# Performance work log

Measured on AMD Instinct MI355X. Metric: run time of the kernel, lower is better.

The kernel has to match this reference:

```python
import jax, jax.numpy as jnp
import numpy as np

NUM_BOXES = 16384
NUM_CLASS = 3
CODE_SIZE = 7
NMS_PRE = 1024
NMS_POST = 512
NMS_THRESH = 0.8
EPS = 1e-8


def _cross(a, b):
    return a[..., 0] * b[..., 1] - a[..., 1] * b[..., 0]


def _bev_corners(b5):
    # b5: (..., 5) = (cx, cy, dx, dy, ry) -> corners (..., 4, 2)
    c, s = jnp.cos(b5[..., 4]), jnp.sin(b5[..., 4])
    off = jnp.array([[0.5, 0.5], [-0.5, 0.5], [-0.5, -0.5], [0.5, -0.5]], dtype=b5.dtype)
    lx = b5[..., 2:3] * off[:, 0]  # (..., 4)
    ly = b5[..., 3:4] * off[:, 1]
    cx = b5[..., 0:1] + lx * c[..., None] - ly * s[..., None]
    cy = b5[..., 1:2] + lx * s[..., None] + ly * c[..., None]
    return jnp.stack([cx, cy], axis=-1)


def _points_in_box(p, b5):
    # p: (..., K, 2), b5: (..., 5) -> (..., K) bool (point inside rotated rect)
    c, s = jnp.cos(b5[..., 4:5]), jnp.sin(b5[..., 4:5])
    rel = p - b5[..., None, 0:2]
    qx = rel[..., 0] * c + rel[..., 1] * s
    qy = -rel[..., 0] * s + rel[..., 1] * c
    return (jnp.abs(qx) <= b5[..., 2:3] * 0.5 + 1e-5) & (jnp.abs(qy) <= b5[..., 3:4] * 0.5 + 1e-5)


def _pairwise_bev_iou(b5):
    # b5: (N, 5) -> (N, N) rotated BEV IoU (matches iou3d nms_gpu's BEV IoU)
    a = b5[:, None, :]
    b = b5[None, :, :]
    ca = _bev_corners(a)  # (N,1,4,2)
    cb = _bev_corners(b)  # (1,N,4,2)
    # edge-edge segment intersections: (N,N,4,4)
    a0, da = ca, jnp.roll(ca, -1, axis=-2) - ca
    b0, db = cb, jnp.roll(cb, -1, axis=-2) - cb
    A0, DA = a0[..., :, None, :], da[..., :, None, :]
    B0, DB = b0[..., None, :, :], db[..., None, :, :]
    den = _cross(DA, DB)
    d = B0 - A0
    den_s = jnp.where(jnp.abs(den) > EPS, den, 1.0)
    t = _cross(d, DB) / den_s
    u = _cross(d, DA) / den_s
    ok = (jnp.abs(den) > EPS) & (t >= 0) & (t <= 1) & (u >= 0) & (u <= 1)
    p_ee = A0 + t[..., None] * DA  # (N,N,4,4,2)
    shp = p_ee.shape[:-3]
    p_ee = p_ee.reshape(shp + (16, 2))
    ok = ok.reshape(shp + (16,))
    in_b = _points_in_box(ca, b)  # corners of A inside B: (N,N,4)
    in_a = _points_in_box(cb, a)  # corners of B inside A: (N,N,4)
    pts = jnp.concatenate([p_ee,
                           jnp.broadcast_to(ca, shp + (4, 2)),
                           jnp.broadcast_to(cb, shp + (4, 2))], axis=-2)  # (N,N,24,2)
    msk = jnp.concatenate([ok, in_b, in_a], axis=-1)  # (N,N,24)
    # order candidate vertices by angle around centroid (intersection is convex)
    cnt = jnp.maximum(msk.sum(-1, keepdims=True), 1)
    ctr = (pts * msk[..., None]).sum(-2, keepdims=True) / cnt[..., None]  # (N,N,1,2)
    ang = jnp.arctan2(pts[..., 1] - ctr[..., 1], pts[..., 0] - ctr[..., 0])
    ang = jnp.where(msk, ang, 1e9)  # invalid points sorted to the end
    order = jnp.argsort(ang, axis=-1)
    pts_s = jnp.take_along_axis(pts, order[..., None], axis=-2)
    msk_s = jnp.take_along_axis(msk, order, axis=-1)
    first = pts_s[..., 0:1, :]
    poly = jnp.where(msk_s[..., None], pts_s, first)  # pad with first vertex (zero shoelace contribution)
    inter = 0.5 * jnp.abs(_cross(poly, jnp.roll(poly, -1, axis=-2)).sum(-1))
    area_a = a[..., 2] * a[..., 3]
    area_b = b[..., 2] * b[..., 3]
    return inter / jnp.maximum(area_a + area_b - inter, 1e-6)


def _greedy_nms(iou, thresh):
    n = iou.shape[0]
    idx = jnp.arange(n)

    def body(i, supp):
        alive = jnp.logical_not(supp[i])
        return supp | (alive & (iou[i] > thresh) & (idx > i))

    supp = jax.lax.fori_loop(0, n, body, jnp.zeros((n,), dtype=bool))
    return ~supp


def _select_one(box_preds, cls_preds):
    # box_preds: (M, 7), cls_preds: (M, C) -> padded selected indices + validity
    scores = jnp.max(cls_preds, axis=1)
    _, top_idx = jax.lax.top_k(scores, NMS_PRE)  # score-descending, like torch.topk
    bev = box_preds[top_idx][:, jnp.array([0, 1, 3, 4, 6])]  # (cx,cy,dx,dy,ry)
    iou = _pairwise_bev_iou(bev)
    keep = _greedy_nms(iou, NMS_THRESH)
    pri = jnp.where(keep, jnp.arange(NMS_PRE), 2 * NMS_PRE)
    pos = jnp.sort(pri)[:NMS_POST]  # kept positions in score order
    valid = pos < NMS_PRE
    sel = top_idx[jnp.minimum(pos, NMS_PRE - 1)]
    return sel, valid


def setup_inputs() -> dict:
    key = jax.random.key(0)
    k1, k2, k3, k4, k5 = jax.random.split(key, 5)
    B = 2
    xy = jax.random.uniform(k1, (B, NUM_BOXES, 2), minval=-50.0, maxval=50.0)
    z = jax.random.uniform(k2, (B, NUM_BOXES, 1), minval=-2.0, maxval=1.0)
    dims = jax.random.uniform(k3, (B, NUM_BOXES, 3), minval=1.0, maxval=5.0)
    ry = jax.random.uniform(k4, (B, NUM_BOXES, 1), minval=-np.pi, maxval=np.pi)
    batch_box_preds = jnp.concatenate([xy, z, dims, ry], axis=-1).astype(jnp.float32)
    batch_cls_preds = (jax.random.normal(k5, (B, NUM_BOXES, NUM_CLASS)) * 3.0).astype(jnp.float32)
    return {"batch_box_preds": batch_box_preds, "batch_cls_preds": batch_cls_preds}


def reference(batch_box_preds, batch_cls_preds):
    # RoIHeadTemplate.proposal_layer: per-sample max-score, class-agnostic NMS,
    # scatter into zero-padded (B, NMS_POST, ...) tensors.
    sel, valid = jax.vmap(_select_one)(batch_box_preds, batch_cls_preds)  # (B, NMS_POST)
    rois = jnp.take_along_axis(batch_box_preds, sel[..., None], axis=1)
    logits = jnp.take_along_axis(batch_cls_preds, sel[..., None], axis=1)
    labels = jnp.argmax(logits, axis=-1)
    scores = jnp.max(logits, axis=-1)
    v = valid[..., None]
    rois = jnp.where(v, rois, 0.0)
    logits = jnp.where(v, logits, 0.0)
    scores = jnp.where(valid, scores, 0.0)
    roi_labels = jnp.where(valid, labels, 0) + 1  # padded slots end up as 1, same as torch (zeros + 1)
    return rois, scores, roi_labels, logits
```

## Files before the change

### kernel.cpp

```cpp
#include <hip/hip_runtime.h>
#include <hip/hip_bf16.h>
#include <math.h>

#define NBOX   16384
#define NPRE   1024
#define NPOST  512
#define NMS_TH 0.8f
#define DEN_EPS 1e-8f
#define NCAND  2048
#define NBUCK  8192
#define SEGCAP 16384
#define CANDL  2048

typedef unsigned long long ull;

__device__ __forceinline__ unsigned mono_f32(float a) {
  unsigned u = __float_as_uint(a);
  return (u & 0x80000000u) ? ~u : (u | 0x80000000u);
}

__global__ __launch_bounds__(256) void k_sel(
    const float* __restrict__ cls, ull* __restrict__ cand,
    unsigned* __restrict__ candCnt) {
  __shared__ unsigned hist[NBUCK];
  __shared__ unsigned smallu[8];
  __shared__ unsigned thrT, cntL;
  const int b = blockIdx.x >> 3, s = blockIdx.x & 7;
  const int t = threadIdx.x;
  const int lane = t & 63, wv = t >> 6;
  const float* cb = cls + (size_t)b * NBOX * 3;

#pragma unroll
  for (int k = 0; k < NBUCK / 256; ++k) hist[t + k * 256] = 0u;
  if (t == 0) cntL = 0u;
  __syncthreads();

  for (int k = 0; k < 64; ++k) {
    int i = k * 256 + t;
    float sc = fmaxf(cb[i * 3], fmaxf(cb[i * 3 + 1], cb[i * 3 + 2]));
    atomicAdd(&hist[mono_f32(sc) >> 19], 1u);
  }
  __syncthreads();

  unsigned csum = 0;
#pragma unroll 8
  for (int k = 0; k < 32; ++k) csum += hist[t * 32 + k];
  unsigned v = csum;
#pragma unroll
  for (int off = 1; off < 64; off <<= 1) {
    unsigned o = __shfl_down((int)v, off, 64);
    if (lane + off < 64) v += o;
  }
  if (lane == 0) smallu[wv] = v;
  __syncthreads();
  unsigned shi = 0;
  for (int w2 = wv + 1; w2 < 4; ++w2) shi += smallu[w2];
  unsigned incl = v + shi;
  unsigned safter = incl - csum;
  if (safter < NPRE && incl >= NPRE) {
    unsigned c = safter;
    for (int k = 31; k >= 0; --k) {
      c += hist[t * 32 + k];
      if (c >= NPRE) { thrT = (unsigned)(t * 32 + k); break; }
    }
  }
  __syncthreads();
  unsigned T = thrT;

  ull* seg = cand + ((size_t)b * 8 + s) * 2048;
  for (int k = s * 8; k < s * 8 + 8; ++k) {
    int i = k * 256 + t;
    float sc = fmaxf(cb[i * 3], fmaxf(cb[i * 3 + 1], cb[i * 3 + 2]));
    unsigned u = mono_f32(sc);
    bool cnd = (u >> 19) >= T;
    ull bal = __ballot(cnd);
    if (bal) {
      unsigned base = 0;
      if (lane == 0) base = atomicAdd(&cntL, (unsigned)__popcll(bal));
      base = (unsigned)__shfl((int)base, 0, 64);
      if (cnd) {
        unsigned pos = base + (unsigned)__popcll(bal & ((1ull << lane) - 1ull));
        seg[pos] = (((ull)u) << 14) | (ull)(16383 - i);
      }
    }
  }
  __syncthreads();
  if (t == 0) candCnt[b * 8 + s] = cntL;
}

__global__ __launch_bounds__(256) void k_rank(
    const float* __restrict__ box, const ull* __restrict__ cand,
    const unsigned* __restrict__ candCnt,
    int* __restrict__ topi, float* __restrict__ binfo, float4* __restrict__ pinfoG) {
  __shared__ ull candL[NCAND];
  __shared__ unsigned offs[9];
  const int b = blockIdx.x >> 3, g = blockIdx.x & 7;
  const int t = threadIdx.x;

  if (t == 0) {
    unsigned o = 0;
    for (int s = 0; s < 8; ++s) {
      offs[s] = o;
      unsigned c = candCnt[b * 8 + s];
      o += (c < 2048u) ? c : 2048u;
    }
    offs[8] = o;
  }
  __syncthreads();
  unsigned C = offs[8]; if (C > NCAND) C = NCAND;
  for (int s = 0; s < 8; ++s) {
    unsigned base = offs[s], cnt = offs[s + 1] - offs[s];
    const ull* seg = cand + ((size_t)b * 8 + s) * 2048;
    for (unsigned e = (unsigned)t; e < cnt; e += 256) {
      unsigned dst = base + e;
      if (dst < NCAND) candL[dst] = seg[e];
    }
  }
  if (t < 2 && C + t < NCAND) candL[C + t] = 0ull;
  __syncthreads();

  int j = g * 256 + t;
  ull my = ((unsigned)j < C) ? candL[j] : 0ull;
  int r = 0;
  int kmax = (int)((C + 1) >> 1);
  const ulonglong2* p2 = (const ulonglong2*)candL;
  for (int k = 0; k < kmax; ++k) {
    ulonglong2 kk = p2[k];
    r += (kk.x > my) ? 1 : 0;
    r += (kk.y > my) ? 1 : 0;
  }
  if ((unsigned)j >= C || r >= NPRE) return;
  int i = 16383 - (int)(my & 0x3FFFULL);
  topi[b * NPRE + r] = i;
  const float* bp = box + ((size_t)b * NBOX + i) * 7;
  float x = bp[0], y = bp[1], dx = bp[3], dy = bp[4], ry = bp[6];
  float c = cosf(ry), s = sinf(ry);
  float* o = binfo + ((size_t)b * NPRE + r) * 16;
  o[0] = x; o[1] = y; o[2] = dx; o[3] = dy; o[4] = c; o[5] = s;
  const float offx[4] = {0.5f, -0.5f, -0.5f, 0.5f};
  const float offy[4] = {0.5f, 0.5f, -0.5f, -0.5f};
#pragma unroll
  for (int k = 0; k < 4; ++k) {
    float lx = dx * offx[k], ly = dy * offy[k];
    o[6 + k]  = x + lx * c - ly * s;
    o[10 + k] = y + lx * s + ly * c;
  }
  float rad = 0.5f * sqrtf(dx * dx + dy * dy);
  float area = dx * dy;
  o[14] = rad; o[15] = area;
  pinfoG[(size_t)b * NPRE + r] = make_float4(x, y, rad, area);
}

__device__ bool iou_exact_gt(const float* __restrict__ Ab, const float* __restrict__ Bb) {
  float ax = Ab[0], ay = Ab[1], bx = Bb[0], by = Bb[1];
  float aA = Ab[15], aB = Bb[15];
  float acx[4], acy[4], bcx[4], bcy[4];
#pragma unroll
  for (int k = 0; k < 4; ++k) {
    acx[k] = Ab[6 + k]; acy[k] = Ab[10 + k];
    bcx[k] = Bb[6 + k]; bcy[k] = Bb[10 + k];
  }
  float px[24], py[24];
  bool act[24];
#pragma unroll
  for (int p = 0; p < 4; ++p) {
    float A0x = acx[p], A0y = acy[p];
    float DAx = acx[(p + 1) & 3] - A0x, DAy = acy[(p + 1) & 3] - A0y;
#pragma unroll
    for (int q = 0; q < 4; ++q) {
      float B0x = bcx[q], B0y = bcy[q];
      float DBx = bcx[(q + 1) & 3] - B0x, DBy = bcy[(q + 1) & 3] - B0y;
      float den = DAx * DBy - DAy * DBx;
      float dxx = B0x - A0x, dyy = B0y - A0y;
      bool dok = fabsf(den) > DEN_EPS;
      float dens = dok ? den : 1.0f;
      float t = (dxx * DBy - dyy * DBx) / dens;
      float u = (dxx * DAy - dyy * DAx) / dens;
      int k = p * 4 + q;
      px[k] = A0x + t * DAx;
      py[k] = A0y + t * DAy;
      act[k] = dok && t >= 0.f && t <= 1.f && u >= 0.f && u <= 1.f;
    }
  }
  float cA = Ab[4], sA = Ab[5], cB = Bb[4], sB = Bb[5];
#pragma unroll
  for (int k = 0; k < 4; ++k) {
    float rx = acx[k] - bx, ry = acy[k] - by;
    float qx =  rx * cB + ry * sB, qy = -rx * sB + ry * cB;
    px[16 + k] = acx[k]; py[16 + k] = acy[k];
    act[16 + k] = (fabsf(qx) <= Bb[2] * 0.5f + 1e-5f) && (fabsf(qy) <= Bb[3] * 0.5f + 1e-5f);
  }
#pragma unroll
  for (int k = 0; k < 4; ++k) {
    float rx = bcx[k] - ax, ry = bcy[k] - ay;
    float qx =  rx * cA + ry * sA, qy = -rx * sA + ry * cA;
    px[20 + k] = bcx[k]; py[20 + k] = bcy[k];
    act[20 + k] = (fabsf(qx) <= Ab[2] * 0.5f + 1e-5f) && (fabsf(qy) <= Ab[3] * 0.5f + 1e-5f);
  }
  int cnt = 0; float sx = 0.f, sy = 0.f;
#pragma unroll
  for (int k = 0; k < 24; ++k)
    if (act[k]) { cnt++; sx += px[k]; sy += py[k]; }
  float fc = (float)(cnt > 1 ? cnt : 1);
  float cx0 = sx / fc, cy0 = sy / fc;
  ull key[24];
#pragma unroll
  for (int k = 0; k < 24; ++k) {
    float ang = atan2f(py[k] - cy0, px[k] - cx0);
    key[k] = act[k] ? ((((ull)mono_f32(ang)) << 5) | (ull)k) : ~0ull;
  }
  ull kmin = ~0ull; float fx = 0.f, fy = 0.f;
#pragma unroll
  for (int k = 0; k < 24; ++k) {
    bool lt = key[k] < kmin;
    kmin = lt ? key[k] : kmin;
    fx = lt ? px[k] : fx;
    fy = lt ? py[k] : fy;
  }
  float ssum = 0.f;
#pragma unroll
  for (int k = 0; k < 24; ++k) {
    ull myk = key[k];
    ull best = ~0ull; float nx = fx, ny = fy;
#pragma unroll
    for (int j = 0; j < 24; ++j) {
      bool c = (key[j] > myk) && (key[j] < best);
      best = c ? key[j] : best;
      nx = c ? px[j] : nx;
      ny = c ? py[j] : ny;
    }
    float contrib = px[k] * ny - py[k] * nx;
    ssum += (myk != ~0ull) ? contrib : 0.f;
  }
  float inter = 0.5f * fabsf(ssum);
  float uni = aA + aB - inter;
  return inter / fmaxf(uni, 1e-6f) > NMS_TH;
}

__global__ __launch_bounds__(256) void k_pairs(
    const float4* __restrict__ pinfoG, const float* __restrict__ binfo,
    unsigned* __restrict__ hitseg, unsigned* __restrict__ hitcnt) {
  __shared__ float4 pin[NPRE];
  __shared__ unsigned candL[CANDL];
  __shared__ unsigned cntC, cntH;
  const int b = blockIdx.x >> 6, blk = blockIdx.x & 63;
  const int t = threadIdx.x;
  const int lane = t & 63, wv = t >> 6;
#pragma unroll
  for (int k = 0; k < 4; ++k) pin[k * 256 + t] = pinfoG[(size_t)b * NPRE + k * 256 + t];
  if (t == 0) { cntC = 0u; cntH = 0u; }
  __syncthreads();

  const float* bi = binfo + (size_t)b * NPRE * 16;
  unsigned sbase = ((unsigned)b * 64 + (unsigned)blk) * SEGCAP;
  for (int iter = 0; iter < 64; ++iter) {
    int task = iter * 4 + wv;
    int q = task >> 4, w = task & 15;
    int i = q * 64 + blk;
    if (w * 64 + 63 <= i) continue;
    int j = w * 64 + lane;
    float4 pi = pin[i];
    float4 pj = pin[j];
    bool cnd = false;
    if (j > i) {
      float ddx = pi.x - pj.x, ddy = pi.y - pj.y;
      float rr = pi.z + pj.z + 1e-3f;
      if (ddx * ddx + ddy * ddy <= rr * rr) {
        float mn = fminf(pi.w, pj.w), mx = fmaxf(pi.w, pj.w);
        if (mn > NMS_TH * mx) cnd = true;
      }
    }
    ull bal = __ballot(cnd);
    if (!bal) continue;
    unsigned base = 0;
    if (lane == 0) base = atomicAdd(&cntC, (unsigned)__popcll(bal));
    base = (unsigned)__shfl((int)base, 0, 64);
    if (cnd) {
      unsigned off = base + (unsigned)__popcll(bal & ((1ull << lane) - 1ull));
      unsigned pk = ((unsigned)i << 10) | (unsigned)j;
      if (off < CANDL) candL[off] = pk;
      else {
        if (iou_exact_gt(bi + (size_t)i * 16, bi + (size_t)j * 16)) {
          unsigned h = atomicAdd(&cntH, 1u);
          hitseg[sbase + h] = pk;
        }
      }
    }
  }
  __syncthreads();

  unsigned C = cntC; if (C > CANDL) C = CANDL;
  for (unsigned e = (unsigned)t; e < C; e += 256) {
    unsigned pk = candL[e];
    unsigned i = pk >> 10, j = pk & 1023u;
    if (iou_exact_gt(bi + (size_t)i * 16, bi + (size_t)j * 16)) {
      unsigned h = atomicAdd(&cntH, 1u);
      hitseg[sbase + h] = pk;
    }
  }
  __syncthreads();
  if (t == 0) hitcnt[b * 64 + blk] = (cntH < (unsigned)SEGCAP) ? cntH : (unsigned)SEGCAP;
}

__device__ __forceinline__ int popbelow(const unsigned* rowbm, int i) {
  int s = 0, w = i >> 5;
  for (int k = 0; k < w; ++k) s += __popc(rowbm[k]);
  s += __popc(rowbm[w] & ((1u << (i & 31)) - 1u));
  return s;
}

__global__ __launch_bounds__(512) void k_fin(
    const float* __restrict__ box, const float* __restrict__ cls,
    const int* __restrict__ topi, const unsigned* __restrict__ hitseg,
    const unsigned* __restrict__ hitcnt, float* __restrict__ out, int B) {
  __shared__ unsigned maskL[128 * 32];
  __shared__ unsigned rlist[NPRE];
  __shared__ unsigned segoff[65];
  __shared__ unsigned rowbm[32];
  __shared__ ull remv_sh[16];
  __shared__ unsigned smallu[8];
  __shared__ unsigned rn_sh;

  const int b = blockIdx.x, t = threadIdx.x;
  const int lane = t & 63, wv = t >> 6;

  for (int k = t; k < 128 * 32; k += 512) maskL[k] = 0u;
  if (t < 32) rowbm[t] = 0u;
  if (t == 0) {
    unsigned o = 0;
    for (int s = 0; s < 64; ++s) {
      segoff[s] = o;
      unsigned c = hitcnt[b * 64 + s];
      o += (c < (unsigned)SEGCAP) ? c : (unsigned)SEGCAP;
    }
    segoff[64] = o;
  }
  __syncthreads();
  unsigned H = segoff[64];

  for (unsigned e = (unsigned)t; e < H; e += 512) {
    int lo = 0, hi = 63;
    while (lo < hi) { int mid = (lo + hi + 1) >> 1; if (segoff[mid] <= e) lo = mid; else hi = mid - 1; }
    unsigned pk = hitseg[((size_t)b * 64 + lo) * SEGCAP + (e - segoff[lo])];
    atomicOr(&rowbm[(pk >> 10) >> 5], 1u << ((pk >> 10) & 31));
  }
  __syncthreads();
  for (int row = t; row < NPRE; row += 512) {
    if ((rowbm[row >> 5] >> (row & 31)) & 1u)
      rlist[popbelow(rowbm, row)] = (unsigned)row;
  }
  if (t == 0) {
    unsigned s = 0;
    for (int w = 0; w < 32; ++w) s += (unsigned)__popc(rowbm[w]);
    rn_sh = s;
  }
  __syncthreads();
  for (unsigned e = (unsigned)t; e < H; e += 512) {
    int lo = 0, hi = 63;
    while (lo < hi) { int mid = (lo + hi + 1) >> 1; if (segoff[mid] <= e) lo = mid; else hi = mid - 1; }
    unsigned pk = hitseg[((size_t)b * 64 + lo) * SEGCAP + (e - segoff[lo])];
    unsigned i = pk >> 10, j = pk & 1023u;
    int slot = popbelow(rowbm, (int)i);
    if (slot < 128) atomicOr(&maskL[slot * 32 + (j >> 5)], 1u << (j & 31));
  }
  __syncthreads();

  if (wv == 0) {
    ull remv = 0;
    unsigned rn = rn_sh;
    for (unsigned s = 0; s < rn; ++s) {
      unsigned row = rlist[s];
      ull m = 0;
      if (s < 128) {
        if (lane < 16)
          m = (ull)maskL[s * 32 + lane * 2] | ((ull)maskL[s * 32 + lane * 2 + 1] << 32);
      } else {
        for (unsigned e = 0; e < H; ++e) {
          int lo = 0, hi = 63;
          while (lo < hi) { int mid = (lo + hi + 1) >> 1; if (segoff[mid] <= e) lo = mid; else hi = mid - 1; }
          unsigned pk = hitseg[((size_t)b * 64 + lo) * SEGCAP + (e - segoff[lo])];
          if ((pk >> 10) == row) {
            unsigned j = pk & 1023u;
            if (lane == (int)(j >> 6)) m |= 1ull << (j & 63);
          }
        }
      }
      ull rw = __shfl(remv, (int)(row >> 6), 64);
      if (!((rw >> (row & 63)) & 1ULL)) remv |= m;
    }
    if (lane < 16) remv_sh[lane] = remv;
  }
  __syncthreads();

  int p0 = t * 2;
  ull rw = remv_sh[p0 >> 6];
  int a0 = ((rw >> (p0 & 63)) & 1ULL) ? 0 : 1;
  int a1 = ((rw >> ((p0 + 1) & 63)) & 1ULL) ? 0 : 1;
  int myc = a0 + a1;
  int v = myc;
#pragma unroll
  for (int off = 1; off < 64; off <<= 1) {
    int t2 = __shfl_up(v, off, 64);
    if (lane >= off) v += t2;
  }
  if (lane == 63) smallu[wv] = (unsigned)v;
  __syncthreads();
  int pre = 0;
  for (int w2 = 0; w2 < wv; ++w2) pre += (int)smallu[w2];
  int total = 0;
  for (int w2 = 0; w2 < 8; ++w2) total += (int)smallu[w2];
  int s = pre + v - myc;

  float* rois   = out;
  float* scores = out + (size_t)B * NPOST * 7;
  float* labels = scores + (size_t)B * NPOST;
  float* logits = labels + (size_t)B * NPOST;
  int aa[2] = {a0, a1};
#pragma unroll
  for (int k = 0; k < 2; ++k) {
    if (aa[k] && s < NPOST) {
      int orig = topi[b * NPRE + p0 + k];
      const float* bb = box + ((size_t)b * NBOX + orig) * 7;
      float* ro = rois + ((size_t)b * NPOST + s) * 7;
#pragma unroll
      for (int c2 = 0; c2 < 7; ++c2) ro[c2] = bb[c2];
      const float* cc = cls + ((size_t)b * NBOX + orig) * 3;
      float l0 = cc[0], l1 = cc[1], l2 = cc[2];
      float m = fmaxf(l0, fmaxf(l1, l2));
      int lab = (l0 == m) ? 0 : ((l1 == m) ? 1 : 2);
      scores[b * NPOST + s] = m;
      labels[b * NPOST + s] = (float)(lab + 1);
      float* lg = logits + ((size_t)b * NPOST + s) * 3;
      lg[0] = l0; lg[1] = l1; lg[2] = l2;
    }
    s += aa[k];
  }
  if (t < NPOST && t >= total) {
    float* ro = rois + ((size_t)b * NPOST + t) * 7;
#pragma unroll
    for (int c2 = 0; c2 < 7; ++c2) ro[c2] = 0.f;
    scores[b * NPOST + t] = 0.f;
    labels[b * NPOST + t] = 1.f;
    float* lg = logits + ((size_t)b * NPOST + t) * 3;
    lg[0] = 0.f; lg[1] = 0.f; lg[2] = 0.f;
  }
}

extern "C" void kernel_launch(void* const* d_in, const int* in_sizes, int n_in,
                              void* d_out, int out_size, void* d_ws, size_t ws_size,
                              hipStream_t stream) {
  const float* box = (const float*)d_in[0];
  const float* cls = (const float*)d_in[1];
  float* out = (float*)d_out;
  int B = in_sizes[0] / (NBOX * 7);

  char* w = (char*)d_ws;
  size_t off = 0;
  ull* cand        = (ull*)(w + off);      off += (size_t)B * 8 * 2048 * sizeof(ull);
  unsigned* candCt = (unsigned*)(w + off); off += (size_t)B * 8 * sizeof(unsigned);
  int* topi        = (int*)(w + off);      off += (size_t)B * NPRE * sizeof(int);
  unsigned* hitcnt = (unsigned*)(w + off); off += (size_t)B * 64 * sizeof(unsigned);
  off = (off + 63) & ~(size_t)63;
  float* binfo     = (float*)(w + off);    off += (size_t)B * NPRE * 16 * sizeof(float);
  float4* pinfoG   = (float4*)(w + off);   off += (size_t)B * NPRE * sizeof(float4);
  unsigned* hitseg = (unsigned*)(w + off); off += (size_t)B * 64 * SEGCAP * sizeof(unsigned);
  (void)off; (void)ws_size; (void)out_size; (void)n_in;

  hipLaunchKernelGGL(k_sel,   dim3(B * 8),  dim3(256), 0, stream, cls, cand, candCt);
  hipLaunchKernelGGL(k_rank,  dim3(B * 8),  dim3(256), 0, stream, box, cand, candCt, topi, binfo, pinfoG);
  hipLaunchKernelGGL(k_pairs, dim3(B * 64), dim3(256), 0, stream, pinfoG, binfo, hitseg, hitcnt);
  hipLaunchKernelGGL(k_fin,   dim3(B),      dim3(512), 0, stream, box, cls, topi, hitseg, hitcnt, out, B);
}
```

Measured before the change: 132.0 us.

## Fuse pair-IoU and final NMS kernels via last-block-done atomic counter

Merges the pairwise IoU kernel and the per-sample finalize kernel into one launch. Each block bumps a per-sample done counter after writing its hit count, and the last block for each sample runs the serial NMS and output scatter, reusing the pair kernel's shared buffers. This removes one kernel launch and the gap between kernels. In exchange the finalize step now runs with 256 threads instead of 512, relies on threadfence ordering, and assumes at most 64 samples because the counter array is fixed at that size.

```diff
diff --git a/kernel.cpp b/kernel.cpp
--- a/kernel.cpp
+++ b/kernel.cpp
@@ -21,7 +21,7 @@
 
 __global__ __launch_bounds__(256) void k_sel(
     const float* __restrict__ cls, ull* __restrict__ cand,
-    unsigned* __restrict__ candCnt) {
+    unsigned* __restrict__ candCnt, unsigned* __restrict__ done) {
   __shared__ unsigned hist[NBUCK];
   __shared__ unsigned smallu[8];
   __shared__ unsigned thrT, cntL;
@@ -30,6 +30,7 @@
   const int lane = t & 63, wv = t >> 6;
   const float* cb = cls + (size_t)b * NBOX * 3;
 
+  if (blockIdx.x == 0 && t < 64) done[t] = 0u;
 #pragma unroll
   for (int k = 0; k < NBUCK / 256; ++k) hist[t + k * 256] = 0u;
   if (t == 0) cntL = 0u;
@@ -237,12 +238,23 @@
   return inter / fmaxf(uni, 1e-6f) > NMS_TH;
 }
 
-__global__ __launch_bounds__(256) void k_pairs(
+__device__ __forceinline__ int popbelow(const unsigned* rowbm, int i) {
+  int s = 0, w = i >> 5;
+  for (int k = 0; k < w; ++k) s += __popc(rowbm[k]);
+  s += __popc(rowbm[w] & ((1u << (i & 31)) - 1u));
+  return s;
+}
+
+__global__ __launch_bounds__(256) void k_pairsfin(
     const float4* __restrict__ pinfoG, const float* __restrict__ binfo,
-    unsigned* __restrict__ hitseg, unsigned* __restrict__ hitcnt) {
+    const float* __restrict__ box, const float* __restrict__ cls,
+    const int* __restrict__ topi,
+    unsigned* __restrict__ hitseg, unsigned* __restrict__ hitcnt,
+    unsigned* __restrict__ done, float* __restrict__ out, int B) {
   __shared__ float4 pin[NPRE];
   __shared__ unsigned candL[CANDL];
   __shared__ unsigned cntC, cntH;
+  __shared__ int amLast;
   const int b = blockIdx.x >> 6, blk = blockIdx.x & 63;
   const int t = threadIdx.x;
   const int lane = t & 63, wv = t >> 6;
@@ -299,32 +311,25 @@
     }
   }
   __syncthreads();
-  if (t == 0) hitcnt[b * 64 + blk] = (cntH < (unsigned)SEGCAP) ? cntH : (unsigned)SEGCAP;
-}
-
-__device__ __forceinline__ int popbelow(const unsigned* rowbm, int i) {
-  int s = 0, w = i >> 5;
-  for (int k = 0; k < w; ++k) s += __popc(rowbm[k]);
-  s += __popc(rowbm[w] & ((1u << (i & 31)) - 1u));
-  return s;
-}
-
-__global__ __launch_bounds__(512) void k_fin(
-    const float* __restrict__ box, const float* __restrict__ cls,
-    const int* __restrict__ topi, const unsigned* __restrict__ hitseg,
-    const unsigned* __restrict__ hitcnt, float* __restrict__ out, int B) {
-  __shared__ unsigned maskL[128 * 32];
-  __shared__ unsigned rlist[NPRE];
+  if (t == 0) {
+    hitcnt[b * 64 + blk] = (cntH < (unsigned)SEGCAP) ? cntH : (unsigned)SEGCAP;
+    __threadfence();
+    unsigned old = atomicAdd(&done[b], 1u);
+    amLast = (old == 63u) ? 1 : 0;
+  }
+  __syncthreads();
+  if (!amLast) return;
+  __threadfence();
+
+  unsigned* maskL = (unsigned*)pin;
+  unsigned* rlist = candL;
   __shared__ unsigned segoff[65];
   __shared__ unsigned rowbm[32];
   __shared__ ull remv_sh[16];
-  __shared__ unsigned smallu[8];
+  __shared__ unsigned smallu[4];
   __shared__ unsigned rn_sh;
 
-  const int b = blockIdx.x, t = threadIdx.x;
-  const int lane = t & 63, wv = t >> 6;
-
-  for (int k = t; k < 128 * 32; k += 512) maskL[k] = 0u;
+  for (int k = t; k < 128 * 32; k += 256) maskL[k] = 0u;
   if (t < 32) rowbm[t] = 0u;
   if (t == 0) {
     unsigned o = 0;
@@ -338,14 +343,14 @@
   __syncthreads();
   unsigned H = segoff[64];
 
-  for (unsigned e = (unsigned)t; e < H; e += 512) {
+  for (unsigned e = (unsigned)t; e < H; e += 256) {
     int lo = 0, hi = 63;
     while (lo < hi) { int mid = (lo + hi + 1) >> 1; if (segoff[mid] <= e) lo = mid; else hi = mid - 1; }
-    unsigned pk = hitseg[((size_t)b * 64 + lo) * SEGCAP + (e - segoff[lo])];
+    unsigned pk = hitseg[((size_t)(b * 64 + lo)) * SEGCAP + (e - segoff[lo])];
     atomicOr(&rowbm[(pk >> 10) >> 5], 1u << ((pk >> 10) & 31));
   }
   __syncthreads();
-  for (int row = t; row < NPRE; row += 512) {
+  for (int row = t; row < NPRE; row += 256) {
     if ((rowbm[row >> 5] >> (row & 31)) & 1u)
       rlist[popbelow(rowbm, row)] = (unsigned)row;
   }
@@ -355,10 +360,10 @@
     rn_sh = s;
   }
   __syncthreads();
-  for (unsigned e = (unsigned)t; e < H; e += 512) {
+  for (unsigned e = (unsigned)t; e < H; e += 256) {
     int lo = 0, hi = 63;
     while (lo < hi) { int mid = (lo + hi + 1) >> 1; if (segoff[mid] <= e) lo = mid; else hi = mid - 1; }
-    unsigned pk = hitseg[((size_t)b * 64 + lo) * SEGCAP + (e - segoff[lo])];
+    unsigned pk = hitseg[((size_t)(b * 64 + lo)) * SEGCAP + (e - segoff[lo])];
     unsigned i = pk >> 10, j = pk & 1023u;
     int slot = popbelow(rowbm, (int)i);
     if (slot < 128) atomicOr(&maskL[slot * 32 + (j >> 5)], 1u << (j & 31));
@@ -378,7 +383,7 @@
         for (unsigned e = 0; e < H; ++e) {
           int lo = 0, hi = 63;
           while (lo < hi) { int mid = (lo + hi + 1) >> 1; if (segoff[mid] <= e) lo = mid; else hi = mid - 1; }
-          unsigned pk = hitseg[((size_t)b * 64 + lo) * SEGCAP + (e - segoff[lo])];
+          unsigned pk = hitseg[((size_t)(b * 64 + lo)) * SEGCAP + (e - segoff[lo])];
           if ((pk >> 10) == row) {
             unsigned j = pk & 1023u;
             if (lane == (int)(j >> 6)) m |= 1ull << (j & 63);
@@ -392,11 +397,13 @@
   }
   __syncthreads();
 
-  int p0 = t * 2;
+  int p0 = t * 4;
   ull rw = remv_sh[p0 >> 6];
-  int a0 = ((rw >> (p0 & 63)) & 1ULL) ? 0 : 1;
+  int a0 = ((rw >> ((p0 + 0) & 63)) & 1ULL) ? 0 : 1;
   int a1 = ((rw >> ((p0 + 1) & 63)) & 1ULL) ? 0 : 1;
-  int myc = a0 + a1;
+  int a2 = ((rw >> ((p0 + 2) & 63)) & 1ULL) ? 0 : 1;
+  int a3 = ((rw >> ((p0 + 3) & 63)) & 1ULL) ? 0 : 1;
+  int myc = a0 + a1 + a2 + a3;
   int v = myc;
 #pragma unroll
   for (int off = 1; off < 64; off <<= 1) {
@@ -407,17 +414,16 @@
   __syncthreads();
   int pre = 0;
   for (int w2 = 0; w2 < wv; ++w2) pre += (int)smallu[w2];
-  int total = 0;
-  for (int w2 = 0; w2 < 8; ++w2) total += (int)smallu[w2];
+  int total = (int)(smallu[0] + smallu[1] + smallu[2] + smallu[3]);
   int s = pre + v - myc;
 
   float* rois   = out;
   float* scores = out + (size_t)B * NPOST * 7;
   float* labels = scores + (size_t)B * NPOST;
   float* logits = labels + (size_t)B * NPOST;
-  int aa[2] = {a0, a1};
-#pragma unroll
-  for (int k = 0; k < 2; ++k) {
+  int aa[4] = {a0, a1, a2, a3};
+#pragma unroll
+  for (int k = 0; k < 4; ++k) {
     if (aa[k] && s < NPOST) {
       int orig = topi[b * NPRE + p0 + k];
       const float* bb = box + ((size_t)b * NBOX + orig) * 7;
@@ -435,14 +441,16 @@
     }
     s += aa[k];
   }
-  if (t < NPOST && t >= total) {
-    float* ro = rois + ((size_t)b * NPOST + t) * 7;
-#pragma unroll
-    for (int c2 = 0; c2 < 7; ++c2) ro[c2] = 0.f;
-    scores[b * NPOST + t] = 0.f;
-    labels[b * NPOST + t] = 1.f;
-    float* lg = logits + ((size_t)b * NPOST + t) * 3;
-    lg[0] = 0.f; lg[1] = 0.f; lg[2] = 0.f;
+  for (int p2 = t; p2 < NPOST; p2 += 256) {
+    if (p2 >= total) {
+      float* ro = rois + ((size_t)b * NPOST + p2) * 7;
+#pragma unroll
+      for (int c2 = 0; c2 < 7; ++c2) ro[c2] = 0.f;
+      scores[b * NPOST + p2] = 0.f;
+      labels[b * NPOST + p2] = 1.f;
+      float* lg = logits + ((size_t)b * NPOST + p2) * 3;
+      lg[0] = 0.f; lg[1] = 0.f; lg[2] = 0.f;
+    }
   }
 }
 
@@ -460,14 +468,15 @@
   unsigned* candCt = (unsigned*)(w + off); off += (size_t)B * 8 * sizeof(unsigned);
   int* topi        = (int*)(w + off);      off += (size_t)B * NPRE * sizeof(int);
   unsigned* hitcnt = (unsigned*)(w + off); off += (size_t)B * 64 * sizeof(unsigned);
+  unsigned* done   = (unsigned*)(w + off); off += 64 * sizeof(unsigned);
   off = (off + 63) & ~(size_t)63;
   float* binfo     = (float*)(w + off);    off += (size_t)B * NPRE * 16 * sizeof(float);
   float4* pinfoG   = (float4*)(w + off);   off += (size_t)B * NPRE * sizeof(float4);
   unsigned* hitseg = (unsigned*)(w + off); off += (size_t)B * 64 * SEGCAP * sizeof(unsigned);
   (void)off; (void)ws_size; (void)out_size; (void)n_in;
 
-  hipLaunchKernelGGL(k_sel,   dim3(B * 8),  dim3(256), 0, stream, cls, cand, candCt);
-  hipLaunchKernelGGL(k_rank,  dim3(B * 8),  dim3(256), 0, stream, box, cand, candCt, topi, binfo, pinfoG);
-  hipLaunchKernelGGL(k_pairs, dim3(B * 64), dim3(256), 0, stream, pinfoG, binfo, hitseg, hitcnt);
-  hipLaunchKernelGGL(k_fin,   dim3(B),      dim3(512), 0, stream, box, cls, topi, hitseg, hitcnt, out, B);
-}
+  hipLaunchKernelGGL(k_sel,      dim3(B * 8),  dim3(256), 0, stream, cls, cand, candCt, done);
+  hipLaunchKernelGGL(k_rank,     dim3(B * 8),  dim3(256), 0, stream, box, cand, candCt, topi, binfo, pinfoG);
+  hipLaunchKernelGGL(k_pairsfin, dim3(B * 64), dim3(256), 0, stream, pinfoG, binfo, box, cls, topi,
+                     hitseg, hitcnt, done, out, B);
+}
```

Result: no change. 133.5 us (+1.1%).
